# Kernel tuning notes

Hardware: AMD Instinct MI355X
Metric: run time of the kernel (lower is better)

Reference implementation:

```python
import jax, jax.numpy as jnp
import numpy as np

SEQ, BATCH, DIM = 2048, 32, 1024


def setup_inputs() -> dict:
    key = jax.random.key(0)
    k1, k2, k3, k4, k5 = jax.random.split(key, 5)
    scale = 1.0 / np.sqrt(DIM)
    return {
        "decoder_hidden": jax.random.normal(k1, (BATCH, 1, DIM), dtype=jnp.float32),
        "encoder_out": jax.random.normal(k2, (SEQ, BATCH, DIM), dtype=jnp.float32),
        "W_enc": jax.random.normal(k3, (DIM, DIM), dtype=jnp.float32) * scale,
        "W_dec": jax.random.normal(k4, (DIM, DIM), dtype=jnp.float32) * scale,
        "V_att": jax.random.normal(k5, (1, DIM), dtype=jnp.float32) * scale,
    }


def reference(decoder_hidden, encoder_out, W_enc, W_dec, V_att):
    # encoder_out: (seq, batch, dim); decoder_hidden: (batch, 1, dim)
    # torch Linear: y = x @ W.T with W of shape (out, in)
    keys = jnp.einsum('sbd,ed->bse', encoder_out, W_enc)      # (batch, seq, dim)
    query = decoder_hidden @ W_dec.T                           # (batch, 1, dim)
    scores = jnp.tanh(keys + query)                            # (batch, seq, dim)
    logits = jnp.einsum('bsd,d->bs', scores, V_att[0])         # (batch, seq)
    alpha = jax.nn.softmax(logits, axis=1)[..., None]          # (batch, seq, 1)
    # context = alpha^T @ encoder_out_permuted -> (batch, 1, dim)
    context = jnp.einsum('bs,sbd->bd', alpha[..., 0], encoder_out)[:, None, :]
    return context, jnp.transpose(alpha, (2, 0, 1))            # (1, batch, seq)
```

## Files before the change

### kernel.cpp

```cpp
#include <hip/hip_runtime.h>
#include <hip/hip_bf16.h>
#include <math.h>

#define SEQ   2048
#define BATCH 32
#define DIM   1024
#define MROWS (SEQ*BATCH)
#define NT2   4
#define NCH   16
#define NKT   32

typedef __attribute__((ext_vector_type(8))) short short8;
typedef __attribute__((ext_vector_type(8))) unsigned short u16x8;
typedef __attribute__((ext_vector_type(4))) float f32x4;

__device__ __forceinline__ unsigned short f2bf(float f) {
  unsigned u = __builtin_bit_cast(unsigned, f);
  u += 0x7FFFu + ((u >> 16) & 1u);
  return (unsigned short)(u >> 16);
}

__device__ __forceinline__ void gl16(const unsigned short* g, unsigned short* l) {
  __builtin_amdgcn_global_load_lds(
      (const __attribute__((address_space(1))) unsigned int*)g,
      (__attribute__((address_space(3))) unsigned int*)l, 16, 0, 0);
}

__global__ __launch_bounds__(256) void conv_bf16_k(const float* __restrict__ src,
                                                   unsigned short* __restrict__ dst) {
  size_t i = ((size_t)blockIdx.x * 256 + threadIdx.x) * 8;
  f32x4 a = __builtin_nontemporal_load(reinterpret_cast<const f32x4*>(src + i));
  f32x4 b = __builtin_nontemporal_load(reinterpret_cast<const f32x4*>(src + i + 4));
  u16x8 o;
  o[0] = f2bf(a[0]); o[1] = f2bf(a[1]); o[2] = f2bf(a[2]); o[3] = f2bf(a[3]);
  o[4] = f2bf(b[0]); o[5] = f2bf(b[1]); o[6] = f2bf(b[2]); o[7] = f2bf(b[3]);
  *reinterpret_cast<u16x8*>(dst + i) = o;
}

__global__ __launch_bounds__(256) void qpart_k(const float* __restrict__ dh,
                                               const float* __restrict__ Wd,
                                               float* __restrict__ qpart) {
  const int bx = blockIdx.x;
  const int eb = bx & 3;
  const int dc = bx >> 2;
  __shared__ float ldh[BATCH][128];
  const int tid = threadIdx.x;
#pragma unroll
  for (int i = 0; i < 4; ++i) {
    int idx = tid + i * 256;
    int bb = idx >> 5, d4 = idx & 31;
    float4 v = *reinterpret_cast<const float4*>(&dh[(size_t)bb * DIM + dc * 128 + d4 * 4]);
    *reinterpret_cast<float4*>(&ldh[bb][d4 * 4]) = v;
  }
  __syncthreads();
  const int e = eb * 256 + tid;
  float acc[BATCH];
#pragma unroll
  for (int b = 0; b < BATCH; ++b) acc[b] = 0.f;
  for (int d4 = 0; d4 < 32; ++d4) {
    float4 w = *reinterpret_cast<const float4*>(&Wd[(size_t)e * DIM + dc * 128 + d4 * 4]);
#pragma unroll
    for (int b = 0; b < BATCH; ++b) {
      float4 h = *reinterpret_cast<const float4*>(&ldh[b][d4 * 4]);
      acc[b] += w.x * h.x + w.y * h.y + w.z * h.z + w.w * h.w;
    }
  }
#pragma unroll
  for (int b = 0; b < BATCH; ++b)
    qpart[((size_t)dc * BATCH + b) * DIM + e] = acc[b];
}

__global__ __launch_bounds__(256) void qred_k(const float* __restrict__ qpart,
                                              float* __restrict__ q) {
  int i = blockIdx.x * 256 + threadIdx.x;
  float s = 0.f;
#pragma unroll
  for (int dc = 0; dc < 8; ++dc) s += qpart[(size_t)dc * 32768 + i];
  q[i] = s;
}

#define BARR  __builtin_amdgcn_s_barrier()
#define VMC(n) asm volatile("s_waitcnt vmcnt(" #n ")" ::: "memory")

#define STAGE_A(t) do {                                                           \
    gl16(Abase + (size_t)lr0 * 1024 + (t) * 32 + cSt * 8,                         \
         (unsigned short*)(arena + (((t) & 3) * 32768)) + w * 512);               \
  } while (0)

#define STAGE_B(t) do {                                                           \
    gl16(Bbase + (size_t)lr0 * 1024 + (t) * 32 + cSt * 8,                         \
         (unsigned short*)(arena + (((t) & 3) * 32768) + 16384) + w * 512);       \
  } while (0)

#define LOAD_AB(d) do {                                                           \
    const char* bA_ = arena + (d) * 32768;                                        \
    const char* bB_ = arena + (d) * 32768 + 16384;                                \
    _Pragma("unroll") for (int i_ = 0; i_ < 4; ++i_) {                            \
      int row_ = wr * 64 + i_ * 16 + fr;                                          \
      int lc_ = kq ^ ((row_ >> 1) & 3);                                           \
      a[i_] = *(const short8*)(bA_ + row_ * 64 + lc_ * 16);                       \
    }                                                                             \
    _Pragma("unroll") for (int j_ = 0; j_ < 4; ++j_) {                            \
      int row_ = wc * 64 + j_ * 16 + fr;                                          \
      int lc_ = kq ^ ((row_ >> 1) & 3);                                           \
      b[j_] = *(const short8*)(bB_ + row_ * 64 + lc_ * 16);                       \
    } } while (0)

#define QUAD() do {                                                               \
    __builtin_amdgcn_s_setprio(1);                                                \
    _Pragma("unroll") for (int i_ = 0; i_ < 4; ++i_)                              \
    _Pragma("unroll") for (int j_ = 0; j_ < 4; ++j_)                              \
      acc[i_][j_] = __builtin_amdgcn_mfma_f32_16x16x32_bf16(                      \
          a[i_], b[j_], acc[i_][j_], 0, 0, 0);                                    \
    __builtin_amdgcn_s_setprio(0);                                                \
  } while (0)

__global__ __launch_bounds__(1024, 4) void gemm8p(const unsigned short* __restrict__ A,
                                                  const unsigned short* __restrict__ B,
                                                  const float* __restrict__ q,
                                                  const float* __restrict__ V,
                                                  float* __restrict__ lpart) {
  __shared__ __align__(16) char arena[131072];

  const int bid = blockIdx.x;
  const int wg = (bid & 7) * 128 + (bid >> 3);
  const int mt = wg >> 2, nt = wg & 3;
  const int row0 = mt * 256, col0 = nt * 256;
  const int tid = threadIdx.x;
  const int lane = tid & 63, w = tid >> 6;
  const int wr = w >> 2, wc = w & 3;
  const int fr = lane & 15, kq = lane >> 4;

  const int lr0 = tid >> 2;
  const int cSt = (tid & 3) ^ ((lr0 >> 1) & 3);

  const unsigned short* Abase = A + (size_t)row0 * DIM;
  const unsigned short* Bbase = B + (size_t)col0 * DIM;

  f32x4 acc[4][4];
#pragma unroll
  for (int i = 0; i < 4; ++i)
#pragma unroll
    for (int j = 0; j < 4; ++j) acc[i][j] = (f32x4)(0.f);

  short8 a[4], b[4];

  STAGE_A(0); STAGE_B(0); STAGE_A(1); STAGE_B(1); STAGE_A(2); STAGE_B(2);
  VMC(4);
  BARR;

#pragma unroll 1
  for (int t = 0; t < NKT - 3; ++t) {
    LOAD_AB(t & 3);
    STAGE_A(t + 3); STAGE_B(t + 3);
    VMC(4);
    BARR; QUAD(); BARR;
  }
  LOAD_AB((NKT - 3) & 3);
  VMC(2);
  BARR; QUAD(); BARR;
  LOAD_AB((NKT - 2) & 3);
  VMC(0);
  BARR; QUAD(); BARR;
  LOAD_AB((NKT - 1) & 3);
  BARR; QUAD(); BARR;

  __syncthreads();
  float* qld = (float*)arena;
  float* vld = (float*)(arena + 33280);
  float* red = (float*)(arena + 34304);
#pragma unroll
  for (int i = 0; i < 2; ++i) {
    int id = i * 1024 + tid;
    int bb = id >> 6, e4 = id & 63;
    float4 v = *(const float4*)&q[(size_t)bb * DIM + col0 + e4 * 4];
    *(float4*)&qld[bb * 260 + e4 * 4] = v;
  }
  if (tid < 64) *(float4*)&vld[tid * 4] = *(const float4*)&V[col0 + tid * 4];
  __syncthreads();

#pragma unroll
  for (int mf = 0; mf < 4; ++mf) {
#pragma unroll
    for (int reg = 0; reg < 4; ++reg) {
      const int m_loc = wr * 64 + mf * 16 + kq * 4 + reg;
      const int bb = m_loc & 31;
      float val = 0.f;
#pragma unroll
      for (int nf = 0; nf < 4; ++nf) {
        const int el = wc * 64 + nf * 16 + fr;
        float x = acc[mf][nf][reg] + qld[bb * 260 + el];
        float g = __expf(2.f * x);
        float tnh = 1.f - 2.f * __builtin_amdgcn_rcpf(g + 1.f);
        val += tnh * vld[el];
      }
      val += __shfl_xor(val, 1); val += __shfl_xor(val, 2);
      val += __shfl_xor(val, 4); val += __shfl_xor(val, 8);
      if (fr == 0) red[wc * 256 + m_loc] = val;
    }
  }
  __syncthreads();
  if (tid < 256) {
    float s = red[tid] + red[256 + tid] + red[512 + tid] + red[768 + tid];
    lpart[(size_t)(row0 + tid) * NT2 + nt] = s;
  }
}

__global__ __launch_bounds__(256) void softmax_k(const float* __restrict__ lpart,
                                                 float* __restrict__ alpha) {
  const int b = blockIdx.x;
  __shared__ float lv[SEQ];
  __shared__ float sred[4];
  const int tid = threadIdx.x;
  float mx = -1e30f;
  for (int s = tid; s < SEQ; s += 256) {
    const float* p = &lpart[(size_t)(s * BATCH + b) * NT2];
    float v = p[0] + p[1] + p[2] + p[3];
    lv[s] = v;
    mx = fmaxf(mx, v);
  }
#pragma unroll
  for (int off = 32; off >= 1; off >>= 1) mx = fmaxf(mx, __shfl_xor(mx, off));
  if ((tid & 63) == 0) sred[tid >> 6] = mx;
  __syncthreads();
  mx = fmaxf(fmaxf(sred[0], sred[1]), fmaxf(sred[2], sred[3]));
  __syncthreads();
  float sm = 0.f;
  for (int s = tid; s < SEQ; s += 256) {
    float e = expf(lv[s] - mx);
    lv[s] = e;
    sm += e;
  }
#pragma unroll
  for (int off = 32; off >= 1; off >>= 1) sm += __shfl_xor(sm, off);
  if ((tid & 63) == 0) sred[tid >> 6] = sm;
  __syncthreads();
  const float inv = 1.f / (sred[0] + sred[1] + sred[2] + sred[3]);
  for (int s = tid; s < SEQ; s += 256)
    alpha[(size_t)b * SEQ + s] = lv[s] * inv;
}

__global__ __launch_bounds__(256) void ctx_part_k(const unsigned short* __restrict__ encbf,
                                                  const float* __restrict__ alpha,
                                                  float* __restrict__ cpart) {
  const int blk = blockIdx.x;
  const int b = blk & 31;
  const int ch = blk >> 5;
  const int tid = threadIdx.x;
  const int g = tid >> 7;
  const int d0 = (tid & 127) * 8;
  const int s0 = ch * (SEQ / NCH);
  float acc8[8];
#pragma unroll
  for (int k = 0; k < 8; ++k) acc8[k] = 0.f;
#pragma unroll 4
  for (int i = 0; i < SEQ / NCH; i += 2) {
    const int s = s0 + i + g;
    const float a = alpha[(size_t)b * SEQ + s];
    u16x8 v = *reinterpret_cast<const u16x8*>(&encbf[((size_t)s * BATCH + b) * DIM + d0]);
#pragma unroll
    for (int k = 0; k < 8; ++k) {
      float f = __builtin_bit_cast(float, (unsigned)v[k] << 16);
      acc8[k] += a * f;
    }
  }
  size_t o = ((size_t)(ch * 2 + g) * BATCH + b) * DIM + d0;
  float4 lo = {acc8[0], acc8[1], acc8[2], acc8[3]};
  float4 hi = {acc8[4], acc8[5], acc8[6], acc8[7]};
  *(float4*)&cpart[o] = lo;
  *(float4*)&cpart[o + 4] = hi;
}

__global__ __launch_bounds__(256) void ctxred_k(const float* __restrict__ cpart,
                                                float* __restrict__ out) {
  int i = blockIdx.x * 256 + threadIdx.x;
  float s = 0.f;
#pragma unroll
  for (int ch = 0; ch < 32; ++ch) s += cpart[(size_t)ch * 32768 + i];
  out[i] = s;
}

extern "C" void kernel_launch(void* const* d_in, const int* in_sizes, int n_in,
                              void* d_out, int out_size, void* d_ws, size_t ws_size,
                              hipStream_t stream) {
  const float* dh   = (const float*)d_in[0];
  const float* enc  = (const float*)d_in[1];
  const float* Wenc = (const float*)d_in[2];
  const float* Wdec = (const float*)d_in[3];
  const float* Vatt = (const float*)d_in[4];
  float* out = (float*)d_out;

  float* ws = (float*)d_ws;
  float* q      = ws;
  float* qpart  = ws + 32768;
  float* lpart  = ws + 294912;
  float* cpart  = ws + 557056;
  unsigned short* Wbf   = (unsigned short*)(ws + 1605632);
  unsigned short* encbf = (unsigned short*)(ws + 2129920);

  conv_bf16_k<<<dim3(512),   dim3(256), 0, stream>>>(Wenc, Wbf);
  qpart_k    <<<dim3(32),    dim3(256), 0, stream>>>(dh, Wdec, qpart);
  qred_k     <<<dim3(128),   dim3(256), 0, stream>>>(qpart, q);
  conv_bf16_k<<<dim3(32768), dim3(256), 0, stream>>>(enc, encbf);
  gemm8p     <<<dim3(1024),  dim3(1024), 0, stream>>>(encbf, Wbf, q, Vatt, lpart);
  softmax_k  <<<dim3(BATCH),     dim3(256), 0, stream>>>(lpart, out + 32768);
  ctx_part_k <<<dim3(BATCH*NCH), dim3(256), 0, stream>>>(encbf, out + 32768, cpart);
  ctxred_k   <<<dim3(128),       dim3(256), 0, stream>>>(cpart, out);
}
```

Measured before the change: 275.2 us.

## Shrink GEMM tile to 256x128 with 512 threads and triple-buffered LDS

Each GEMM block now covers 256x128 output columns with 8 waves instead of 256x256 with 16 waves, so twice as many blocks launch and the N dimension splits into 8 partial logits. The LDS pipeline goes from four stages to three, shrinking shared memory from 128KB to 72KB so more blocks can be resident per CU. Softmax now sums 8 partials per row and the workspace offsets move to fit the larger lpart. The cost is less reuse of A tiles, since each encoder row tile is loaded by 8 blocks instead of 4, and a shallower prefetch depth.

```diff
diff --git a/kernel.cpp b/kernel.cpp
--- a/kernel.cpp
+++ b/kernel.cpp
@@ -6,7 +6,7 @@
 #define BATCH 32
 #define DIM   1024
 #define MROWS (SEQ*BATCH)
-#define NT2   4
+#define NT2   8
 #define NCH   16
 #define NKT   32
 
@@ -82,19 +82,19 @@
 #define BARR  __builtin_amdgcn_s_barrier()
 #define VMC(n) asm volatile("s_waitcnt vmcnt(" #n ")" ::: "memory")
 
-#define STAGE_A(t) do {                                                           \
-    gl16(Abase + (size_t)lr0 * 1024 + (t) * 32 + cSt * 8,                         \
-         (unsigned short*)(arena + (((t) & 3) * 32768)) + w * 512);               \
+#define STAGE(t) do {                                                             \
+    const int bo_ = ((t) % 3) * 24576;                                            \
+    gl16(Abase + (size_t)rA0 * 1024 + (t) * 32 + cA0 * 8,                         \
+         (unsigned short*)(arena + bo_) + w * 512);                               \
+    gl16(Abase + (size_t)(rA0 + 128) * 1024 + (t) * 32 + cA0 * 8,                 \
+         (unsigned short*)(arena + bo_ + 8192) + w * 512);                        \
+    gl16(Bbase + (size_t)rB0 * 1024 + (t) * 32 + cB0 * 8,                         \
+         (unsigned short*)(arena + bo_ + 16384) + w * 512);                       \
   } while (0)
 
-#define STAGE_B(t) do {                                                           \
-    gl16(Bbase + (size_t)lr0 * 1024 + (t) * 32 + cSt * 8,                         \
-         (unsigned short*)(arena + (((t) & 3) * 32768) + 16384) + w * 512);       \
-  } while (0)
-
 #define LOAD_AB(d) do {                                                           \
-    const char* bA_ = arena + (d) * 32768;                                        \
-    const char* bB_ = arena + (d) * 32768 + 16384;                                \
+    const char* bA_ = arena + (d) * 24576;                                        \
+    const char* bB_ = arena + (d) * 24576 + 16384;                                \
     _Pragma("unroll") for (int i_ = 0; i_ < 4; ++i_) {                            \
       int row_ = wr * 64 + i_ * 16 + fr;                                          \
       int lc_ = kq ^ ((row_ >> 1) & 3);                                           \
@@ -115,24 +115,26 @@
     __builtin_amdgcn_s_setprio(0);                                                \
   } while (0)
 
-__global__ __launch_bounds__(1024, 4) void gemm8p(const unsigned short* __restrict__ A,
-                                                  const unsigned short* __restrict__ B,
-                                                  const float* __restrict__ q,
-                                                  const float* __restrict__ V,
-                                                  float* __restrict__ lpart) {
-  __shared__ __align__(16) char arena[131072];
+__global__ __launch_bounds__(512, 4) void gemm8p(const unsigned short* __restrict__ A,
+                                                 const unsigned short* __restrict__ B,
+                                                 const float* __restrict__ q,
+                                                 const float* __restrict__ V,
+                                                 float* __restrict__ lpart) {
+  __shared__ __align__(16) char arena[73728];
 
   const int bid = blockIdx.x;
-  const int wg = (bid & 7) * 128 + (bid >> 3);
-  const int mt = wg >> 2, nt = wg & 3;
-  const int row0 = mt * 256, col0 = nt * 256;
+  const int wg = (bid & 7) * 256 + (bid >> 3);
+  const int mt = wg >> 3, nt = wg & 7;
+  const int row0 = mt * 256, col0 = nt * 128;
   const int tid = threadIdx.x;
   const int lane = tid & 63, w = tid >> 6;
-  const int wr = w >> 2, wc = w & 3;
+  const int wr = w >> 1, wc = w & 1;
   const int fr = lane & 15, kq = lane >> 4;
 
-  const int lr0 = tid >> 2;
-  const int cSt = (tid & 3) ^ ((lr0 >> 1) & 3);
+  const int rA0 = tid >> 2;
+  const int cA0 = (tid & 3) ^ ((rA0 >> 1) & 3);
+  const int rB0 = tid >> 2;
+  const int cB0 = cA0;
 
   const unsigned short* Abase = A + (size_t)row0 * DIM;
   const unsigned short* Bbase = B + (size_t)col0 * DIM;
@@ -145,38 +147,35 @@
 
   short8 a[4], b[4];
 
-  STAGE_A(0); STAGE_B(0); STAGE_A(1); STAGE_B(1); STAGE_A(2); STAGE_B(2);
-  VMC(4);
+  STAGE(0); STAGE(1);
+  VMC(3);
   BARR;
 
 #pragma unroll 1
-  for (int t = 0; t < NKT - 3; ++t) {
-    LOAD_AB(t & 3);
-    STAGE_A(t + 3); STAGE_B(t + 3);
-    VMC(4);
+  for (int t = 0; t < NKT - 2; ++t) {
+    LOAD_AB(t % 3);
+    STAGE(t + 2);
+    VMC(3);
     BARR; QUAD(); BARR;
   }
-  LOAD_AB((NKT - 3) & 3);
-  VMC(2);
-  BARR; QUAD(); BARR;
-  LOAD_AB((NKT - 2) & 3);
+  LOAD_AB((NKT - 2) % 3);
   VMC(0);
   BARR; QUAD(); BARR;
-  LOAD_AB((NKT - 1) & 3);
+  LOAD_AB((NKT - 1) % 3);
   BARR; QUAD(); BARR;
 
   __syncthreads();
   float* qld = (float*)arena;
-  float* vld = (float*)(arena + 33280);
-  float* red = (float*)(arena + 34304);
+  float* vld = (float*)(arena + 16896);
+  float* red = (float*)(arena + 17408);
 #pragma unroll
   for (int i = 0; i < 2; ++i) {
-    int id = i * 1024 + tid;
-    int bb = id >> 6, e4 = id & 63;
+    int id = i * 512 + tid;
+    int bb = id >> 5, e4 = id & 31;
     float4 v = *(const float4*)&q[(size_t)bb * DIM + col0 + e4 * 4];
-    *(float4*)&qld[bb * 260 + e4 * 4] = v;
-  }
-  if (tid < 64) *(float4*)&vld[tid * 4] = *(const float4*)&V[col0 + tid * 4];
+    *(float4*)&qld[bb * 132 + e4 * 4] = v;
+  }
+  if (tid < 32) *(float4*)&vld[tid * 4] = *(const float4*)&V[col0 + tid * 4];
   __syncthreads();
 
 #pragma unroll
@@ -189,7 +188,7 @@
 #pragma unroll
       for (int nf = 0; nf < 4; ++nf) {
         const int el = wc * 64 + nf * 16 + fr;
-        float x = acc[mf][nf][reg] + qld[bb * 260 + el];
+        float x = acc[mf][nf][reg] + qld[bb * 132 + el];
         float g = __expf(2.f * x);
         float tnh = 1.f - 2.f * __builtin_amdgcn_rcpf(g + 1.f);
         val += tnh * vld[el];
@@ -201,7 +200,7 @@
   }
   __syncthreads();
   if (tid < 256) {
-    float s = red[tid] + red[256 + tid] + red[512 + tid] + red[768 + tid];
+    float s = red[tid] + red[256 + tid];
     lpart[(size_t)(row0 + tid) * NT2 + nt] = s;
   }
 }
@@ -215,7 +214,7 @@
   float mx = -1e30f;
   for (int s = tid; s < SEQ; s += 256) {
     const float* p = &lpart[(size_t)(s * BATCH + b) * NT2];
-    float v = p[0] + p[1] + p[2] + p[3];
+    float v = ((p[0] + p[1]) + (p[2] + p[3])) + ((p[4] + p[5]) + (p[6] + p[7]));
     lv[s] = v;
     mx = fmaxf(mx, v);
   }
@@ -294,15 +293,15 @@
   float* q      = ws;
   float* qpart  = ws + 32768;
   float* lpart  = ws + 294912;
-  float* cpart  = ws + 557056;
-  unsigned short* Wbf   = (unsigned short*)(ws + 1605632);
-  unsigned short* encbf = (unsigned short*)(ws + 2129920);
+  float* cpart  = ws + 819200;
+  unsigned short* Wbf   = (unsigned short*)(ws + 1867776);
+  unsigned short* encbf = (unsigned short*)(ws + 2392064);
 
   conv_bf16_k<<<dim3(512),   dim3(256), 0, stream>>>(Wenc, Wbf);
   qpart_k    <<<dim3(32),    dim3(256), 0, stream>>>(dh, Wdec, qpart);
   qred_k     <<<dim3(128),   dim3(256), 0, stream>>>(qpart, q);
   conv_bf16_k<<<dim3(32768), dim3(256), 0, stream>>>(enc, encbf);
-  gemm8p     <<<dim3(1024),  dim3(1024), 0, stream>>>(encbf, Wbf, q, Vatt, lpart);
+  gemm8p     <<<dim3(2048),  dim3(512), 0, stream>>>(encbf, Wbf, q, Vatt, lpart);
   softmax_k  <<<dim3(BATCH),     dim3(256), 0, stream>>>(lpart, out + 32768);
   ctx_part_k <<<dim3(BATCH*NCH), dim3(256), 0, stream>>>(encbf, out + 32768, cpart);
   ctxred_k   <<<dim3(128),       dim3(256), 0, stream>>>(cpart, out);
```

Measured after the change: 281.2 us. +2.2%, slower.
